# Kernel tuning notes

Measured on AMD Instinct MI355X. Metric: run time of the kernel, lower is better.

The kernel has to match this reference:

```python
import jax, jax.numpy as jnp
import numpy as np

B, M, D, OUT = 16384, 4096, 512, 128


def setup_inputs() -> dict:
    key = jax.random.key(0)
    ks = jax.random.split(key, 5)
    x = jax.random.normal(ks[0], (B, D), dtype=jnp.float32)
    support = jax.random.normal(ks[1], (M, D), dtype=jnp.float32)
    gamma = jnp.float32(1.0)
    head_w = jax.random.normal(ks[2], (OUT, M), dtype=jnp.float32) / np.sqrt(M)
    head_b = jax.random.normal(ks[3], (OUT,), dtype=jnp.float32) * 0.01
    scale = jnp.ones((1,), dtype=jnp.float32)
    shift = jnp.zeros((1,), dtype=jnp.float32)
    return {"x": x, "support": support, "gamma": gamma,
            "head_w": head_w, "head_b": head_b,
            "scale": scale, "shift": shift}


def reference(x, support, gamma, head_w, head_b, scale, shift):
    x2 = jnp.sum(x * x, axis=-1, keepdims=True)           # [B, 1]
    s2 = jnp.sum(support * support, axis=-1)              # [M]
    xs = jnp.einsum('bd,md->bm', x, support)              # [B, M]
    sqdist = jnp.maximum(x2 + s2[None, :] - 2.0 * xs, 0.0)
    k = jnp.exp(-gamma * sqdist)                          # RBF kernel [B, M]
    out = jnp.einsum('bm,om->bo', k, head_w) + head_b     # linear head [B, OUT]
    return scale * out + shift
```

## Files before the change

### kernel.cpp

```cpp
#include <hip/hip_runtime.h>

typedef unsigned int u32;
typedef unsigned short u16;
typedef unsigned char u8;
typedef __attribute__((ext_vector_type(8))) __bf16 bf16x8;
typedef __attribute__((ext_vector_type(4))) float f32x4;
typedef __attribute__((ext_vector_type(4))) int i32x4;

#define NB 16384
#define NM 4096
#define ND 512
#define NOUT 128
#define L2E 1.44269504088896340736f


#define WAITLG(N) do { asm volatile("s_waitcnt vmcnt(" #N ") lgkmcnt(0)" ::: "memory"); \
                       __builtin_amdgcn_sched_barrier(0); } while (0)
#define SB0() __builtin_amdgcn_sched_barrier(0)

__device__ __forceinline__ u16 f2bf(float f) {
  u32 u = __float_as_uint(f);
  u += 0x7FFFu + ((u >> 16) & 1u);
  return (u16)(u >> 16);
}

__device__ __forceinline__ u8 f2fp8(float f) {
  u32 u = __float_as_uint(f);
  u32 s = (u >> 24) & 0x80u;
  u32 au = u & 0x7FFFFFFFu;
  if (au < 0x3C800000u) return (u8)s;
  au += 0x000FFFFFu + ((au >> 20) & 1u);
  u32 e = (au >> 23) - 120u;
  u32 m = (au >> 20) & 7u;
  return (u8)(s | (e << 3) | m);
}

__device__ __forceinline__ void stage16(const void* g, void* l) {
  __builtin_amdgcn_global_load_lds((__attribute__((address_space(1))) void*)g,
                                   (__attribute__((address_space(3))) void*)l,
                                   16, 0, 0);
}

__device__ __forceinline__ bf16x8 ldg_b128(const void* p) {
  i32x4 r;
  asm volatile("global_load_dwordx4 %0, %1, off" : "=&v"(r) : "v"(p) : "memory");
  return __builtin_bit_cast(bf16x8, r);
}

__device__ __forceinline__ uint4 pack8bf(float4 v0, float4 v1) {
  uint4 pk;
  pk.x = (u32)f2bf(v0.x) | ((u32)f2bf(v0.y) << 16);
  pk.y = (u32)f2bf(v0.z) | ((u32)f2bf(v0.w) << 16);
  pk.z = (u32)f2bf(v1.x) | ((u32)f2bf(v1.y) << 16);
  pk.w = (u32)f2bf(v1.z) | ((u32)f2bf(v1.w) << 16);
  return pk;
}

__device__ __forceinline__ uint2 pack8f8(float4 v0, float4 v1) {
  uint2 pk;
  pk.x = (u32)f2fp8(v0.x) | ((u32)f2fp8(v0.y) << 8) |
         ((u32)f2fp8(v0.z) << 16) | ((u32)f2fp8(v0.w) << 24);
  pk.y = (u32)f2fp8(v1.x) | ((u32)f2fp8(v1.y) << 8) |
         ((u32)f2fp8(v1.z) << 16) | ((u32)f2fp8(v1.w) << 24);
  return pk;
}

__global__ __launch_bounds__(256) void prep_all(const float* __restrict__ x,
                                                const float* __restrict__ s,
                                                const float* __restrict__ hw,
                                                const float* __restrict__ gamma_p,
                                                u8*  __restrict__ x_ws,
                                                u8*  __restrict__ s_ws,
                                                u16* __restrict__ hw_ws,
                                                float* __restrict__ x2g,
                                                float* __restrict__ s2g,
                                                float* __restrict__ out) {
  __shared__ uint2 t8[2048];
  __shared__ uint4 t16[2048];
  const int tid = threadIdx.x, bid = blockIdx.x;
  const int lane = tid & 63, w = tid >> 6;

  if (bid < 640) {
    const bool isx = bid < 512;
    const int blk = isx ? bid : (bid - 512);
    const float* src_m = isx ? x : s;
    u8*    dst_ws = isx ? x_ws : s_ws;
    float* sq_out = isx ? x2g : s2g;
    const float gl   = gamma_p[0] * L2E;
    const float cmul = isx ? 1.0f : (-2.0f * gl);
    const int big  = isx ? (blk >> 1) : (blk >> 2);
    const int roff = isx ? ((blk & 1) * 32) : ((blk & 3) * 32);
    const int rows = isx ? 64 : 128;

    #pragma unroll
    for (int p = 0; p < 8; ++p) {
      const int row = p * 4 + w;
      const float* src = src_m + (size_t)(blk * 32 + row) * ND + lane * 8;
      float4 v0 = *(const float4*)src;
      float4 v1 = *(const float4*)(src + 4);
      float ss = v0.x*v0.x + v0.y*v0.y + v0.z*v0.z + v0.w*v0.w
               + v1.x*v1.x + v1.y*v1.y + v1.z*v1.z + v1.w*v1.w;
      #pragma unroll
      for (int off = 32; off > 0; off >>= 1) ss += __shfl_down(ss, off);
      if (lane == 0) sq_out[blk * 32 + row] = gl * ss;
      v0.x *= cmul; v0.y *= cmul; v0.z *= cmul; v0.w *= cmul;
      v1.x *= cmul; v1.y *= cmul; v1.z *= cmul; v1.w *= cmul;
      t8[lane * 32 + ((row + lane) & 31)] = pack8f8(v0, v1);
    }
    __syncthreads();
    #pragma unroll
    for (int p = 0; p < 8; ++p) {
      const int kg = p * 8 + (tid >> 5);
      const int row = tid & 31;
      uint2 pk = t8[kg * 32 + ((row + kg) & 31)];
      *(uint2*)&dst_ws[(((size_t)(big * 64 + kg)) * rows + roff + row) * 8] = pk;
    }
  } else if (bid < 672) {
    const int blk = bid - 640;
    #pragma unroll
    for (int p = 0; p < 8; ++p) {
      const int o = p * 16 + (tid >> 4);
      const int kg = tid & 15;
      const float* src = hw + (size_t)o * NM + blk * 128 + kg * 8;
      float4 v0 = *(const float4*)src;
      float4 v1 = *(const float4*)(src + 4);
      t16[o * 16 + ((kg + o) & 15)] = pack8bf(v0, v1);
    }
    __syncthreads();
    #pragma unroll
    for (int it = 0; it < 8; ++it) {
      const int kg = it * 2 + (tid >> 7);
      const int o = tid & 127;
      uint4 pk = t16[o * 16 + ((kg + o) & 15)];
      *(uint4*)&hw_ws[(((size_t)(blk * 16 + kg)) * 128 + o) * 8] = pk;
    }
  } else {
    float4* o4 = (float4*)out;
    const float4 z = {0.f, 0.f, 0.f, 0.f};
    size_t base = (size_t)(bid - 672) * 8192 + tid;
    #pragma unroll 8
    for (int i = 0; i < 32; ++i) o4[base + (size_t)i * 256] = z;
  }
}

__global__ __launch_bounds__(256, 2)
void rbf_fused(const u8* __restrict__ x_ws, const u8* __restrict__ s_ws,
               const u16* __restrict__ hw_ws, const float* __restrict__ x2g,
               const float* __restrict__ s2g, const float* __restrict__ head_b,
               const float* __restrict__ scale_p, const float* __restrict__ shift_p,
               float* __restrict__ out)
{
  extern __shared__ __align__(16) char smem[];

  const int tid  = threadIdx.x;
  const int w    = tid >> 6;
  const int lane = tid & 63;
  const int quad = lane >> 4;
  const int l16  = lane & 15;
  const int wr   = w & 1;
  const int wc   = w >> 1;
  const int xcd  = blockIdx.x & 7;
  const int rb   = (blockIdx.x >> 3) * 2 + (xcd & 1);
  const int half = xcd >> 1;
  const int b0   = rb * 64;

  const float vscale = scale_p[0];
  const float vshift = shift_p[0];

  const u8* xsrc = x_ws + (size_t)rb * 32768;
  const u8* ssrc = s_ws + (size_t)(half * 8) * 65536;

  auto stage_grp = [&](int mt_s, int grp_s) {
    const u8* sp = ssrc + (size_t)mt_s * 65536 + grp_s * 8192;
    char* dp = smem + 32768 + (grp_s & 3) * 8192;
    stage16(sp + tid * 16, dp + tid * 16);
    stage16(sp + 4096 + tid * 16, dp + 4096 + tid * 16);
  };

  f32x4 x2v[2];
  #pragma unroll
  for (int r = 0; r < 2; ++r)
    x2v[r] = *(const f32x4*)&x2g[b0 + wr * 32 + r * 16 + quad * 4];
  SB0();
  #pragma unroll
  for (int i = 0; i < 8; ++i)
    stage16(xsrc + i * 4096 + tid * 16, smem + i * 4096 + tid * 16);
  SB0();
  stage_grp(0, 0); SB0();
  stage_grp(0, 1); SB0();
  stage_grp(0, 2);
  asm volatile("s_waitcnt vmcnt(2)" ::: "memory");
  SB0();
  __builtin_amdgcn_s_barrier();
  SB0();

  long long aF[2][2][2];
  long long bF[2][2][4];
  bf16x8 b2[2][4];
  bf16x8 a2h[4][2];

  #pragma unroll
  for (int k2 = 0; k2 < 2; ++k2) {
    #pragma unroll
    for (int r = 0; r < 2; ++r)
      aF[0][k2][r] = *(const long long*)(smem + ((k2 * 4 + quad) * 64 + wr * 32 + r * 16 + l16) * 8);
    #pragma unroll
    for (int c = 0; c < 4; ++c)
      bF[0][k2][c] = *(const long long*)(smem + 32768 +
                       ((k2 * 4 + quad) * 128 + wc * 64 + c * 16 + l16) * 8);
  }
  asm volatile("s_waitcnt lgkmcnt(0)" ::: "memory");
  SB0();

  const f32x4 zf = {0.f, 0.f, 0.f, 0.f};
  f32x4 acc_xs[2][4];
  f32x4 acc_out[2][4];
  #pragma unroll
  for (int r = 0; r < 2; ++r)
    #pragma unroll
    for (int c = 0; c < 4; ++c) { acc_xs[r][c] = zf; acc_out[r][c] = zf; }

  #pragma unroll 1
  for (int mt = 0; mt < 8; ++mt) {
    const int mtg = half * 8 + mt;

    if (mt > 0) {
      #pragma unroll
      for (int ks = 0; ks < 4; ++ks) {
        const int kg = ks * 4 + quad;
        #pragma unroll
        for (int r = 0; r < 2; ++r)
          a2h[ks][r] = *(const bf16x8*)(smem + 65536 + (kg * 64 + wr * 32 + r * 16 + l16) * 16);
      }
      asm volatile("s_waitcnt lgkmcnt(0)" ::: "memory");
      SB0();
    }
    float s2v[4];
    #pragma unroll
    for (int c = 0; c < 4; ++c)
      s2v[c] = s2g[mtg * 128 + wc * 64 + c * 16 + l16];
    SB0();

    #pragma unroll
    for (int grp = 0; grp < 8; ++grp) {
      const int p  = grp & 1;
      const int pn = p ^ 1;
      const int gN = grp + 1;
      const bool doRd = !(mt == 7 && grp == 7);

      __builtin_amdgcn_s_setprio(1);
      #pragma unroll
      for (int r = 0; r < 2; ++r)
        #pragma unroll
        for (int c = 0; c < 4; ++c)
          acc_xs[r][c] = __builtin_amdgcn_mfma_f32_16x16x32_fp8_fp8(
              aF[p][0][r], bF[p][0][c], acc_xs[r][c], 0, 0, 0);
      __builtin_amdgcn_s_setprio(0);
      SB0();
      if (doRd) {
        #pragma unroll
        for (int k2 = 0; k2 < 2; ++k2)
          #pragma unroll
          for (int r = 0; r < 2; ++r)
            aF[pn][k2][r] = *(const long long*)(smem +
                ((((gN & 7) * 2 + k2) * 4 + quad) * 64 + wr * 32 + r * 16 + l16) * 8);
        #pragma unroll
        for (int c = 0; c < 2; ++c)
          bF[pn][0][c] = *(const long long*)(smem + 32768 + (gN & 3) * 8192 +
              ((0 * 4 + quad) * 128 + wc * 64 + c * 16 + l16) * 8);
      }
      SB0();
      __builtin_amdgcn_s_setprio(1);
      #pragma unroll
      for (int r = 0; r < 2; ++r)
        #pragma unroll
        for (int c = 0; c < 4; ++c)
          acc_xs[r][c] = __builtin_amdgcn_mfma_f32_16x16x32_fp8_fp8(
              aF[p][1][r], bF[p][1][c], acc_xs[r][c], 0, 0, 0);
      __builtin_amdgcn_s_setprio(0);
      SB0();
      if (doRd) {
        #pragma unroll
        for (int c = 2; c < 4; ++c)
          bF[pn][0][c] = *(const long long*)(smem + 32768 + (gN & 3) * 8192 +
              ((0 * 4 + quad) * 128 + wc * 64 + c * 16 + l16) * 8);
        #pragma unroll
        for (int c = 0; c < 4; ++c)
          bF[pn][1][c] = *(const long long*)(smem + 32768 + (gN & 3) * 8192 +
              ((1 * 4 + quad) * 128 + wc * 64 + c * 16 + l16) * 8);
      }
      SB0();
      if (mt > 0 && (grp & 1) == 0) {
        __builtin_amdgcn_s_setprio(1);
        #pragma unroll
        for (int r = 0; r < 2; ++r)
          #pragma unroll
          for (int c = 0; c < 4; ++c)
            acc_out[r][c] = __builtin_amdgcn_mfma_f32_16x16x32_bf16(
                a2h[grp >> 1][r], b2[(grp >> 1) & 1][c], acc_out[r][c], 0, 0, 0);
        __builtin_amdgcn_s_setprio(0);
      }
      SB0();
      if (grp <= 4)     stage_grp(mt, grp + 3);
      else if (mt < 7)  stage_grp(mt + 1, grp - 5);
      if ((grp & 1) == 0 && !(mt == 7 && grp == 6)) {
        const int gs = (grp + 2) & 7;
        const int ms = mt + (grp == 6);
        int sl = half * 8 + ms - 1; if (sl < 0) sl = 0;
        const int kg = (gs >> 1) * 4 + quad;
        const size_t sb = (size_t)(sl * 16 + kg);
        #pragma unroll
        for (int c = 0; c < 4; ++c)
          b2[((grp >> 1) + 1) & 1][c] = ldg_b128(hw_ws + (sb * 128 + wc * 64 + c * 16 + l16) * 8);
      }

      if (mt == 7 && grp >= 5)   WAITLG(0);
      else if ((grp & 1) == 0)   WAITLG(6);
      else                       WAITLG(2);
      __builtin_amdgcn_s_barrier();
      SB0();
    }

    {
      #pragma unroll
      for (int r = 0; r < 2; ++r)
        #pragma unroll
        for (int c = 0; c < 4; ++c) {
          const int cl = wc * 64 + c * 16 + l16;
          char* kbase = smem + 65536 + (cl >> 3) * 1024 + (cl & 7) * 2;
          #pragma unroll
          for (int i = 0; i < 4; ++i) {
            const int row = wr * 32 + r * 16 + quad * 4 + i;
            const float t = acc_xs[r][c][i] + x2v[r][i] + s2v[c];
            float kv = __builtin_amdgcn_exp2f(-t);
            kv = fminf(kv, 1.0f);
            *(u16*)(kbase + row * 16) = (u16)(__float_as_uint(kv) >> 16);
            acc_xs[r][c][i] = 0.0f;
          }
        }
    }
    asm volatile("s_waitcnt lgkmcnt(0)" ::: "memory");
    SB0();
    __builtin_amdgcn_s_barrier();
    SB0();
  }

  #pragma unroll
  for (int ks = 0; ks < 4; ++ks) {
    const int kg = ks * 4 + quad;
    const size_t sb = (size_t)((half * 8 + 7) * 16 + kg);
    bf16x8 bb[4], a2[2];
    #pragma unroll
    for (int c = 0; c < 4; ++c)
      bb[c] = *(const bf16x8*)(hw_ws + (sb * 128 + wc * 64 + c * 16 + l16) * 8);
    #pragma unroll
    for (int r = 0; r < 2; ++r)
      a2[r] = *(const bf16x8*)(smem + 65536 + (kg * 64 + wr * 32 + r * 16 + l16) * 16);
    #pragma unroll
    for (int r = 0; r < 2; ++r)
      #pragma unroll
      for (int c = 0; c < 4; ++c)
        acc_out[r][c] = __builtin_amdgcn_mfma_f32_16x16x32_bf16(a2[r], bb[c], acc_out[r][c], 0, 0, 0);
  }

  float addv[4];
  #pragma unroll
  for (int c = 0; c < 4; ++c) {
    const int col = wc * 64 + c * 16 + l16;
    addv[c] = (half == 0) ? (vscale * head_b[col] + vshift) : 0.0f;
  }
  #pragma unroll
  for (int r = 0; r < 2; ++r)
    #pragma unroll
    for (int c = 0; c < 4; ++c) {
      const int col = wc * 64 + c * 16 + l16;
      #pragma unroll
      for (int i = 0; i < 4; ++i) {
        const int row = b0 + wr * 32 + r * 16 + quad * 4 + i;
        atomicAdd(&out[(size_t)row * NOUT + col], vscale * acc_out[r][c][i] + addv[c]);
      }
    }
}

extern "C" void kernel_launch(void* const* d_in, const int* in_sizes, int n_in,
                              void* d_out, int out_size, void* d_ws, size_t ws_size,
                              hipStream_t stream) {
  const float* x       = (const float*)d_in[0];
  const float* support = (const float*)d_in[1];
  const float* gamma   = (const float*)d_in[2];
  const float* head_w  = (const float*)d_in[3];
  const float* head_b  = (const float*)d_in[4];
  const float* scale   = (const float*)d_in[5];
  const float* shift   = (const float*)d_in[6];
  float* out = (float*)d_out;

  char* w = (char*)d_ws;
  u8*    x_ws  = (u8*)(w);
  u8*    s_ws  = (u8*)(w + 8388608);
  u16*   hw_ws = (u16*)(w + 10485760);
  float* x2g   = (float*)(w + 11534336);
  float* s2g   = (float*)(w + 11599872);

  static bool lds_init = false;
  if (!lds_init) {
    hipFuncSetAttribute(reinterpret_cast<const void*>(rbf_fused),
                        hipFuncAttributeMaxDynamicSharedMemorySize, 81920);
    lds_init = true;
  }

  prep_all<<<736, 256, 0, stream>>>(x, support, head_w, gamma,
                                    x_ws, s_ws, hw_ws, x2g, s2g, out);
  rbf_fused<<<1024, 256, 81920, stream>>>(x_ws, s_ws, hw_ws, x2g, s2g,
                                          head_b, scale, shift, out);
}
```

Baseline: 182.3 us.

## Keep x fragments in registers and deepen support-tile staging ring

Each wave now loads its full x A-fragments (16 k-chunks) straight from global memory into registers once, instead of staging x into shared memory and re-reading it every group. That frees the first 64KB of LDS, which now holds an 8-slot ring of support tiles staged two tiles ahead per step. The inner loop is restructured into 4 steps of 4 MFMA k-chunks, with head-weight B fragments and kernel-value reads interleaved per step and new vmcnt wait counts. This removes repeated LDS reads of A but raises register pressure, which may lower occupancy, and adds more LDS wait points.

```diff
diff --git a/kernel.cpp b/kernel.cpp
--- a/kernel.cpp
+++ b/kernel.cpp
@@ -16,6 +16,8 @@
 
 #define WAITLG(N) do { asm volatile("s_waitcnt vmcnt(" #N ") lgkmcnt(0)" ::: "memory"); \
                        __builtin_amdgcn_sched_barrier(0); } while (0)
+#define LGKM0() do { asm volatile("s_waitcnt lgkmcnt(0)" ::: "memory"); \
+                     __builtin_amdgcn_sched_barrier(0); } while (0)
 #define SB0() __builtin_amdgcn_sched_barrier(0)
 
 __device__ __forceinline__ u16 f2bf(float f) {
@@ -170,47 +172,42 @@
   const u8* xsrc = x_ws + (size_t)rb * 32768;
   const u8* ssrc = s_ws + (size_t)(half * 8) * 65536;
 
-  auto stage_grp = [&](int mt_s, int grp_s) {
-    const u8* sp = ssrc + (size_t)mt_s * 65536 + grp_s * 8192;
-    char* dp = smem + 32768 + (grp_s & 3) * 8192;
+  auto stage_tile = [&](int j) {
+    const u8* sp = ssrc + (size_t)(j >> 3) * 65536 + (j & 7) * 8192;
+    char* dp = smem + (j & 7) * 8192;
     stage16(sp + tid * 16, dp + tid * 16);
     stage16(sp + 4096 + tid * 16, dp + 4096 + tid * 16);
   };
 
+  auto rdB = [&](int buf, int kcL, long long* dst) {
+    #pragma unroll
+    for (int c = 0; c < 4; ++c)
+      dst[c] = *(const long long*)(smem + buf * 8192 +
+                ((kcL * 4 + quad) * 128 + wc * 64 + c * 16 + l16) * 8);
+  };
+
   f32x4 x2v[2];
   #pragma unroll
   for (int r = 0; r < 2; ++r)
     x2v[r] = *(const f32x4*)&x2g[b0 + wr * 32 + r * 16 + quad * 4];
   SB0();
-  #pragma unroll
-  for (int i = 0; i < 8; ++i)
-    stage16(xsrc + i * 4096 + tid * 16, smem + i * 4096 + tid * 16);
+  long long aX[16][2];
+  #pragma unroll
+  for (int kc = 0; kc < 16; ++kc)
+    #pragma unroll
+    for (int r = 0; r < 2; ++r)
+      aX[kc][r] = *(const long long*)(xsrc + ((kc * 4 + quad) * 64 + wr * 32 + r * 16 + l16) * 8);
   SB0();
-  stage_grp(0, 0); SB0();
-  stage_grp(0, 1); SB0();
-  stage_grp(0, 2);
-  asm volatile("s_waitcnt vmcnt(2)" ::: "memory");
+  #pragma unroll
+  for (int j = 0; j < 6; ++j) stage_tile(j);
+  asm volatile("s_waitcnt vmcnt(6)" ::: "memory");
   SB0();
   __builtin_amdgcn_s_barrier();
   SB0();
 
-  long long aF[2][2][2];
-  long long bF[2][2][4];
-  bf16x8 b2[2][4];
-  bf16x8 a2h[4][2];
-
-  #pragma unroll
-  for (int k2 = 0; k2 < 2; ++k2) {
-    #pragma unroll
-    for (int r = 0; r < 2; ++r)
-      aF[0][k2][r] = *(const long long*)(smem + ((k2 * 4 + quad) * 64 + wr * 32 + r * 16 + l16) * 8);
-    #pragma unroll
-    for (int c = 0; c < 4; ++c)
-      bF[0][k2][c] = *(const long long*)(smem + 32768 +
-                       ((k2 * 4 + quad) * 128 + wc * 64 + c * 16 + l16) * 8);
-  }
-  asm volatile("s_waitcnt lgkmcnt(0)" ::: "memory");
-  SB0();
+  long long bF0[4], bF1[4];
+  rdB(0, 0, bF0);
+  LGKM0();
 
   const f32x4 zf = {0.f, 0.f, 0.f, 0.f};
   f32x4 acc_xs[2][4];
@@ -220,33 +217,40 @@
     #pragma unroll
     for (int c = 0; c < 4; ++c) { acc_xs[r][c] = zf; acc_out[r][c] = zf; }
 
+  bf16x8 b2[2][4];
+
   #pragma unroll 1
   for (int mt = 0; mt < 8; ++mt) {
     const int mtg = half * 8 + mt;
-
-    if (mt > 0) {
-      #pragma unroll
-      for (int ks = 0; ks < 4; ++ks) {
-        const int kg = ks * 4 + quad;
+    float s2v[4];
+
+    #pragma unroll
+    for (int s = 0; s < 4; ++s) {
+      if (s == 0) {
+        #pragma unroll
+        for (int c = 0; c < 4; ++c)
+          s2v[c] = s2g[mtg * 128 + wc * 64 + c * 16 + l16];
+        SB0();
+      }
+      bf16x8 a2[2];
+
+      __builtin_amdgcn_s_setprio(1);
+      #pragma unroll
+      for (int r = 0; r < 2; ++r)
+        #pragma unroll
+        for (int c = 0; c < 4; ++c)
+          acc_xs[r][c] = __builtin_amdgcn_mfma_f32_16x16x32_fp8_fp8(
+              aX[s * 4 + 0][r], bF0[c], acc_xs[r][c], 0, 0, 0);
+      __builtin_amdgcn_s_setprio(0);
+      SB0();
+      rdB(2 * s, 1, bF1);
+      if (mt > 0) {
+        const int kg = s * 4 + quad;
         #pragma unroll
         for (int r = 0; r < 2; ++r)
-          a2h[ks][r] = *(const bf16x8*)(smem + 65536 + (kg * 64 + wr * 32 + r * 16 + l16) * 16);
-      }
-      asm volatile("s_waitcnt lgkmcnt(0)" ::: "memory");
-      SB0();
-    }
-    float s2v[4];
-    #pragma unroll
-    for (int c = 0; c < 4; ++c)
-      s2v[c] = s2g[mtg * 128 + wc * 64 + c * 16 + l16];
-    SB0();
-
-    #pragma unroll
-    for (int grp = 0; grp < 8; ++grp) {
-      const int p  = grp & 1;
-      const int pn = p ^ 1;
-      const int gN = grp + 1;
-      const bool doRd = !(mt == 7 && grp == 7);
+          a2[r] = *(const bf16x8*)(smem + 65536 + (kg * 64 + wr * 32 + r * 16 + l16) * 16);
+      }
+      LGKM0();
 
       __builtin_amdgcn_s_setprio(1);
       #pragma unroll
@@ -254,69 +258,67 @@
         #pragma unroll
         for (int c = 0; c < 4; ++c)
           acc_xs[r][c] = __builtin_amdgcn_mfma_f32_16x16x32_fp8_fp8(
-              aF[p][0][r], bF[p][0][c], acc_xs[r][c], 0, 0, 0);
+              aX[s * 4 + 1][r], bF1[c], acc_xs[r][c], 0, 0, 0);
       __builtin_amdgcn_s_setprio(0);
       SB0();
-      if (doRd) {
-        #pragma unroll
-        for (int k2 = 0; k2 < 2; ++k2)
-          #pragma unroll
-          for (int r = 0; r < 2; ++r)
-            aF[pn][k2][r] = *(const long long*)(smem +
-                ((((gN & 7) * 2 + k2) * 4 + quad) * 64 + wr * 32 + r * 16 + l16) * 8);
-        #pragma unroll
-        for (int c = 0; c < 2; ++c)
-          bF[pn][0][c] = *(const long long*)(smem + 32768 + (gN & 3) * 8192 +
-              ((0 * 4 + quad) * 128 + wc * 64 + c * 16 + l16) * 8);
-      }
-      SB0();
+      rdB(2 * s + 1, 0, bF0);
+      LGKM0();
+
       __builtin_amdgcn_s_setprio(1);
       #pragma unroll
       for (int r = 0; r < 2; ++r)
         #pragma unroll
         for (int c = 0; c < 4; ++c)
           acc_xs[r][c] = __builtin_amdgcn_mfma_f32_16x16x32_fp8_fp8(
-              aF[p][1][r], bF[p][1][c], acc_xs[r][c], 0, 0, 0);
+              aX[s * 4 + 2][r], bF0[c], acc_xs[r][c], 0, 0, 0);
       __builtin_amdgcn_s_setprio(0);
       SB0();
-      if (doRd) {
-        #pragma unroll
-        for (int c = 2; c < 4; ++c)
-          bF[pn][0][c] = *(const long long*)(smem + 32768 + (gN & 3) * 8192 +
-              ((0 * 4 + quad) * 128 + wc * 64 + c * 16 + l16) * 8);
-        #pragma unroll
-        for (int c = 0; c < 4; ++c)
-          bF[pn][1][c] = *(const long long*)(smem + 32768 + (gN & 3) * 8192 +
-              ((1 * 4 + quad) * 128 + wc * 64 + c * 16 + l16) * 8);
-      }
-      SB0();
-      if (mt > 0 && (grp & 1) == 0) {
+      rdB(2 * s + 1, 1, bF1);
+      LGKM0();
+
+      __builtin_amdgcn_s_setprio(1);
+      #pragma unroll
+      for (int r = 0; r < 2; ++r)
+        #pragma unroll
+        for (int c = 0; c < 4; ++c)
+          acc_xs[r][c] = __builtin_amdgcn_mfma_f32_16x16x32_fp8_fp8(
+              aX[s * 4 + 3][r], bF1[c], acc_xs[r][c], 0, 0, 0);
+      __builtin_amdgcn_s_setprio(0);
+      SB0();
+      if (!(mt == 7 && s == 3)) rdB((2 * s + 2) & 7, 0, bF0);
+      LGKM0();
+
+      if (mt > 0) {
         __builtin_amdgcn_s_setprio(1);
         #pragma unroll
         for (int r = 0; r < 2; ++r)
           #pragma unroll
           for (int c = 0; c < 4; ++c)
             acc_out[r][c] = __builtin_amdgcn_mfma_f32_16x16x32_bf16(
-                a2h[grp >> 1][r], b2[(grp >> 1) & 1][c], acc_out[r][c], 0, 0, 0);
+                a2[r], b2[s & 1][c], acc_out[r][c], 0, 0, 0);
         __builtin_amdgcn_s_setprio(0);
       }
       SB0();
-      if (grp <= 4)     stage_grp(mt, grp + 3);
-      else if (mt < 7)  stage_grp(mt + 1, grp - 5);
-      if ((grp & 1) == 0 && !(mt == 7 && grp == 6)) {
-        const int gs = (grp + 2) & 7;
-        const int ms = mt + (grp == 6);
-        int sl = half * 8 + ms - 1; if (sl < 0) sl = 0;
-        const int kg = (gs >> 1) * 4 + quad;
-        const size_t sb = (size_t)(sl * 16 + kg);
-        #pragma unroll
-        for (int c = 0; c < 4; ++c)
-          b2[((grp >> 1) + 1) & 1][c] = ldg_b128(hw_ws + (sb * 128 + wc * 64 + c * 16 + l16) * 8);
-      }
-
-      if (mt == 7 && grp >= 5)   WAITLG(0);
-      else if ((grp & 1) == 0)   WAITLG(6);
-      else                       WAITLG(2);
+
+      if (s == 0 || mt < 7) {
+        const int j = mt * 8 + 2 * s + 6;
+        stage_tile(j);
+        stage_tile(j + 1);
+      }
+      SB0();
+
+      if ((s <= 1) ? (mt >= 1) : (mt <= 6)) {
+        const int umt = mt + (s >= 2);
+        const int us  = (s + 2) & 3;
+        const size_t sb = (size_t)((half * 8 + umt - 1) * 16 + us * 4 + quad);
+        #pragma unroll
+        for (int c = 0; c < 4; ++c)
+          b2[s & 1][c] = ldg_b128(hw_ws + (sb * 128 + wc * 64 + c * 16 + l16) * 8);
+      }
+
+      if (mt == 0)      { if (s == 0) WAITLG(10); else if (s == 1) WAITLG(4); else WAITLG(8); }
+      else if (mt < 7)  { if (s == 0) WAITLG(12); else WAITLG(8); }
+      else              { if (s == 0) WAITLG(12); else if (s == 1) WAITLG(4); else WAITLG(0); }
       __builtin_amdgcn_s_barrier();
       SB0();
     }
@@ -339,8 +341,7 @@
           }
         }
     }
-    asm volatile("s_waitcnt lgkmcnt(0)" ::: "memory");
-    SB0();
+    LGKM0();
     __builtin_amdgcn_s_barrier();
     SB0();
   }
```

Measured after the change: 187.9 us. 3.0% more time.

## Batch staging into pairs per group and halve block barriers in main loop

Applied to the files above, without the earlier changes.

Restructures the inner group loop so global-to-shared staging and head-weight prefetches are issued two groups at a time at the start of even groups. The workgroup barrier and full vmcnt wait now run only on odd groups rather than every group. The goal is fewer barriers and more MFMA work between syncs. In exchange it drains all outstanding global loads to zero at each barrier, which can expose memory latency that the old partial vmcnt waits hid.

```diff
diff --git a/kernel.cpp b/kernel.cpp
--- a/kernel.cpp
+++ b/kernel.cpp
@@ -16,6 +16,8 @@
 
 #define WAITLG(N) do { asm volatile("s_waitcnt vmcnt(" #N ") lgkmcnt(0)" ::: "memory"); \
                        __builtin_amdgcn_sched_barrier(0); } while (0)
+#define LGKM(N) do { asm volatile("s_waitcnt lgkmcnt(" #N ")" ::: "memory"); \
+                     __builtin_amdgcn_sched_barrier(0); } while (0)
 #define SB0() __builtin_amdgcn_sched_barrier(0)
 
 __device__ __forceinline__ u16 f2bf(float f) {
@@ -189,8 +191,7 @@
   stage_grp(0, 0); SB0();
   stage_grp(0, 1); SB0();
   stage_grp(0, 2);
-  asm volatile("s_waitcnt vmcnt(2)" ::: "memory");
-  SB0();
+  WAITLG(0);
   __builtin_amdgcn_s_barrier();
   SB0();
 
@@ -209,7 +210,8 @@
       bF[0][k2][c] = *(const long long*)(smem + 32768 +
                        ((k2 * 4 + quad) * 128 + wc * 64 + c * 16 + l16) * 8);
   }
-  asm volatile("s_waitcnt lgkmcnt(0)" ::: "memory");
+  LGKM(0);
+  __builtin_amdgcn_s_barrier();
   SB0();
 
   const f32x4 zf = {0.f, 0.f, 0.f, 0.f};
@@ -232,14 +234,9 @@
         for (int r = 0; r < 2; ++r)
           a2h[ks][r] = *(const bf16x8*)(smem + 65536 + (kg * 64 + wr * 32 + r * 16 + l16) * 16);
       }
-      asm volatile("s_waitcnt lgkmcnt(0)" ::: "memory");
-      SB0();
+      LGKM(0);
     }
     float s2v[4];
-    #pragma unroll
-    for (int c = 0; c < 4; ++c)
-      s2v[c] = s2g[mtg * 128 + wc * 64 + c * 16 + l16];
-    SB0();
 
     #pragma unroll
     for (int grp = 0; grp < 8; ++grp) {
@@ -247,6 +244,29 @@
       const int pn = p ^ 1;
       const int gN = grp + 1;
       const bool doRd = !(mt == 7 && grp == 7);
+
+      if ((grp & 1) == 0) {
+        if (grp == 0) {
+          #pragma unroll
+          for (int c = 0; c < 4; ++c)
+            s2v[c] = s2g[mtg * 128 + wc * 64 + c * 16 + l16];
+          SB0();
+        }
+        if (grp == 0)      { stage_grp(mt, 3); stage_grp(mt, 4); }
+        else if (grp == 2) { stage_grp(mt, 5); stage_grp(mt, 6); }
+        else if (grp == 4) { stage_grp(mt, 7); if (mt < 7) stage_grp(mt + 1, 0); }
+        else               { if (mt < 7) { stage_grp(mt + 1, 1); stage_grp(mt + 1, 2); } }
+        SB0();
+        if ((grp < 6 && mt >= 1) || (grp == 6 && mt <= 6)) {
+          const int um = mt + (grp == 6);
+          const int ks = ((grp >> 1) + 1) & 3;
+          const size_t sb = (size_t)((half * 8 + um - 1) * 16 + ks * 4 + quad);
+          #pragma unroll
+          for (int c = 0; c < 4; ++c)
+            b2[((grp >> 1) + 1) & 1][c] = ldg_b128(hw_ws + (sb * 128 + wc * 64 + c * 16 + l16) * 8);
+        }
+        SB0();
+      }
 
       __builtin_amdgcn_s_setprio(1);
       #pragma unroll
@@ -270,6 +290,7 @@
               ((0 * 4 + quad) * 128 + wc * 64 + c * 16 + l16) * 8);
       }
       SB0();
+
       __builtin_amdgcn_s_setprio(1);
       #pragma unroll
       for (int r = 0; r < 2; ++r)
@@ -290,35 +311,24 @@
               ((1 * 4 + quad) * 128 + wc * 64 + c * 16 + l16) * 8);
       }
       SB0();
-      if (mt > 0 && (grp & 1) == 0) {
-        __builtin_amdgcn_s_setprio(1);
-        #pragma unroll
-        for (int r = 0; r < 2; ++r)
+
+      if ((grp & 1) == 0) {
+        if (mt > 0) {
+          __builtin_amdgcn_s_setprio(1);
           #pragma unroll
-          for (int c = 0; c < 4; ++c)
-            acc_out[r][c] = __builtin_amdgcn_mfma_f32_16x16x32_bf16(
-                a2h[grp >> 1][r], b2[(grp >> 1) & 1][c], acc_out[r][c], 0, 0, 0);
-        __builtin_amdgcn_s_setprio(0);
-      }
-      SB0();
-      if (grp <= 4)     stage_grp(mt, grp + 3);
-      else if (mt < 7)  stage_grp(mt + 1, grp - 5);
-      if ((grp & 1) == 0 && !(mt == 7 && grp == 6)) {
-        const int gs = (grp + 2) & 7;
-        const int ms = mt + (grp == 6);
-        int sl = half * 8 + ms - 1; if (sl < 0) sl = 0;
-        const int kg = (gs >> 1) * 4 + quad;
-        const size_t sb = (size_t)(sl * 16 + kg);
-        #pragma unroll
-        for (int c = 0; c < 4; ++c)
-          b2[((grp >> 1) + 1) & 1][c] = ldg_b128(hw_ws + (sb * 128 + wc * 64 + c * 16 + l16) * 8);
-      }
-
-      if (mt == 7 && grp >= 5)   WAITLG(0);
-      else if ((grp & 1) == 0)   WAITLG(6);
-      else                       WAITLG(2);
-      __builtin_amdgcn_s_barrier();
-      SB0();
+          for (int r = 0; r < 2; ++r)
+            #pragma unroll
+            for (int c = 0; c < 4; ++c)
+              acc_out[r][c] = __builtin_amdgcn_mfma_f32_16x16x32_bf16(
+                  a2h[grp >> 1][r], b2[(grp >> 1) & 1][c], acc_out[r][c], 0, 0, 0);
+          __builtin_amdgcn_s_setprio(0);
+        }
+        LGKM(0);
+      } else {
+        WAITLG(0);
+        __builtin_amdgcn_s_barrier();
+        SB0();
+      }
     }
 
     {
@@ -339,8 +349,7 @@
           }
         }
     }
-    asm volatile("s_waitcnt lgkmcnt(0)" ::: "memory");
-    SB0();
+    LGKM(0);
     __builtin_amdgcn_s_barrier();
     SB0();
   }
@@ -349,18 +358,18 @@
   for (int ks = 0; ks < 4; ++ks) {
     const int kg = ks * 4 + quad;
     const size_t sb = (size_t)((half * 8 + 7) * 16 + kg);
-    bf16x8 bb[4], a2[2];
+    bf16x8 bb[4], aa[2];
     #pragma unroll
     for (int c = 0; c < 4; ++c)
       bb[c] = *(const bf16x8*)(hw_ws + (sb * 128 + wc * 64 + c * 16 + l16) * 8);
     #pragma unroll
     for (int r = 0; r < 2; ++r)
-      a2[r] = *(const bf16x8*)(smem + 65536 + (kg * 64 + wr * 32 + r * 16 + l16) * 16);
+      aa[r] = *(const bf16x8*)(smem + 65536 + (kg * 64 + wr * 32 + r * 16 + l16) * 16);
     #pragma unroll
     for (int r = 0; r < 2; ++r)
       #pragma unroll
       for (int c = 0; c < 4; ++c)
-        acc_out[r][c] = __builtin_amdgcn_mfma_f32_16x16x32_bf16(a2[r], bb[c], acc_out[r][c], 0, 0, 0);
+        acc_out[r][c] = __builtin_amdgcn_mfma_f32_16x16x32_bf16(aa[r], bb[c], acc_out[r][c], 0, 0, 0);
   }
 
   float addv[4];
```

After: 182.3 us. Within noise of the previous version (-0.0%).
